# Kernel tuning notes

Measured on AMD Instinct MI355X. Metric: run time of the kernel, lower is better.

## Reference

```python
import jax, jax.numpy as jnp
from jax import lax
import numpy as np

# Model hyper-parameters (from init_kwargs)
B = 4
POINT_NUM = 32768
SKP_NUM = 512
ISK_NUM = 2
K1 = 32                       # skp_neighbor_num
K2 = int(K1 * SKP_NUM * 4 / POINT_NUM)   # = 2, as computed in __init__
RADIUS_SCALING = 1.5
SPHERE_N = 128                # points per sphere template


def _fibonacci_sphere(n):
    i = np.arange(n, dtype=np.float64) + 0.5
    phi = np.arccos(1.0 - 2.0 * i / n)
    theta = np.pi * (1.0 + 5.0 ** 0.5) * i
    return np.stack([np.cos(theta) * np.sin(phi),
                     np.sin(theta) * np.sin(phi),
                     np.cos(phi)], axis=-1).astype(np.float32)


def setup_inputs() -> dict:
    key = jax.random.key(0)
    xyz = jax.random.normal(key, (B, POINT_NUM, 3), dtype=jnp.float32)
    sphere_template = jnp.asarray(_fibonacci_sphere(SPHERE_N))  # [S,3] unit sphere
    return {"xyz": xyz, "sphere_template": sphere_template}


def _fps(xyz, n):
    """Iterative furthest point sampling. xyz: [B,N,3] -> indices [B,n] int32."""
    b, N, _ = xyz.shape
    dist0 = jnp.full((b, N), 1e10, dtype=xyz.dtype)
    last0 = jnp.zeros((b,), dtype=jnp.int32)

    def step(carry, _):
        dist, last = carry
        lp = jnp.take_along_axis(xyz, last[:, None, None], axis=1)  # [B,1,3]
        d = jnp.sum((xyz - lp) ** 2, axis=-1)                        # [B,N]
        dist = jnp.minimum(dist, d)
        nxt = jnp.argmax(dist, axis=-1).astype(jnp.int32)
        return (dist, nxt), last

    (_, _), idxs = lax.scan(step, (dist0, last0), None, length=n)
    return idxs.T  # [B,n]


def _pairwise_sqdist(centers, pts):
    # [B,M,N] squared distances
    c2 = jnp.sum(centers ** 2, axis=-1)[:, :, None]
    p2 = jnp.sum(pts ** 2, axis=-1)[:, None, :]
    cp = jnp.einsum('bmd,bnd->bmn', centers, pts)
    return c2 + p2 - 2.0 * cp


def _sklnz(centers, pts, k):
    """SkeletonizationBlock: move each center to the mean of its k nearest
    points in pts; radius = mean distance to those neighbors."""
    d2 = _pairwise_sqdist(centers, pts)          # [B,M,N]
    neg, idx = lax.top_k(-d2, k)                 # [B,M,k]
    nb = jax.vmap(lambda x, i: x[i])(pts, idx)   # [B,M,k,3]
    new_centers = jnp.mean(nb, axis=2)
    radius = jnp.mean(jnp.sqrt(jnp.clip(-neg, 0.0)), axis=2)  # [B,M]
    return new_centers, radius


def _forward(xyz, sphere_template):
    # Stage 1: FPS to 4*skp_num seeds, then iterative skeletonization
    ids = _fps(xyz, SKP_NUM * 4)                               # [B,4*skp]
    centers = jnp.take_along_axis(xyz, ids[:, :, None], axis=1)
    radius = None
    for _ in range(ISK_NUM):
        centers, radius = _sklnz(centers, xyz, K1)
    # Stage 2: FPS on intermediate skeleton down to skp_num
    xyz2 = centers
    ids2 = _fps(xyz2, SKP_NUM)                                 # [B,skp]
    centers = jnp.take_along_axis(xyz2, ids2[:, :, None], axis=1)
    radius = jnp.take_along_axis(radius, ids2, axis=1)
    for _ in range(ISK_NUM):
        centers, _radius = _sklnz(centers, xyz2, K2)
    radius = (radius + _radius) * RADIUS_SCALING               # [B,skp]
    # Sphere reconstruction: template scaled by radius, translated to centers
    sphere_points = centers[:, :, None, :] + radius[:, :, None, None] * sphere_template[None, None]
    return centers, sphere_points, radius


def reference(xyz, sphere_template):
    return _forward(xyz, sphere_template)
```

## Files before the change

kernel.cpp:

```cpp
#include <hip/hip_runtime.h>
#include <cstdint>

#define BATCH 4
#define NPTS  32768
#define QN    8192
#define SKP   512
#define M1    (SKP*4)
#define KA    32
#define KB    2
#define SPHN  128

typedef unsigned long long u64;

__device__ __forceinline__ float sqdist(float px, float py, float pz,
                                        float cx, float cy, float cz) {
  float dx = px - cx, dy = py - cy, dz = pz - cz;
  return __fadd_rn(__fadd_rn(__fmul_rn(dx, dx), __fmul_rn(dy, dy)),
                   __fmul_rn(dz, dz));
}
__device__ __forceinline__ float d2gram(float px, float py, float pz,
                                        float qx, float qy, float qz, float q2) {
  float p2 = __fadd_rn(__fadd_rn(__fmul_rn(px, px), __fmul_rn(py, py)),
                       __fmul_rn(pz, pz));
  float cp = __fadd_rn(__fadd_rn(__fmul_rn(qx, px), __fmul_rn(qy, py)),
                       __fmul_rn(qz, pz));
  return __fsub_rn(__fadd_rn(q2, p2), __fadd_rn(cp, cp));
}

__device__ __forceinline__ u64 shfl_xor_u64(u64 v, int off) {
  int lo = __shfl_xor((int)(unsigned)v, off);
  int hi = __shfl_xor((int)(unsigned)(v >> 32), off);
  return ((u64)(unsigned)hi << 32) | (unsigned)lo;
}
__device__ __forceinline__ u64 shfl_u64(u64 v, int src) {
  int lo = __shfl((int)(unsigned)v, src);
  int hi = __shfl((int)(unsigned)(v >> 32), src);
  return ((u64)(unsigned)hi << 32) | (unsigned)lo;
}
__device__ __forceinline__ u64 umax64(u64 a, u64 b) { return a > b ? a : b; }
__device__ __forceinline__ u64 umin64(u64 a, u64 b) { return a < b ? a : b; }
__device__ __forceinline__ void ins3(u64& k1, u64& k2, u64& k3, u64 v) {
  k3 = umax64(k3, umin64(k2, v));
  k2 = umax64(k2, umin64(k1, v));
  k1 = umax64(k1, v);
}

__global__ __launch_bounds__(1024)
void fps1_kernel(const float* __restrict__ xyz, float4* __restrict__ cen4a,
                 u64* __restrict__ sync)
{
  int blk = blockIdx.x;
  int b = blk >> 2, sub = blk & 3;
  const float* X = xyz + (size_t)b * NPTS * 3;
  cen4a += (size_t)b * M1;
  int tid = threadIdx.x, lane = tid & 63, wave = tid >> 6;
  int base = sub * QN;

  __shared__ float2 xysh[QN];
  __shared__ u64 s_w[16][8];
  __shared__ float4 s_cc[448];
  __shared__ float s_pivc[48][3];
  __shared__ int s_J;

  float zr[8], dist[8];
#pragma unroll
  for (int j = 0; j < 8; ++j) {
    int pl = tid + 1024 * j;
    int pg = base + pl;
    xysh[pl] = make_float2(X[3*pg], X[3*pg+1]);
    zr[j] = X[3*pg+2];
    dist[j] = 1e10f;
  }
  if (tid == 0) {
    s_pivc[0][0] = X[0]; s_pivc[0][1] = X[1]; s_pivc[0][2] = X[2];
    if (sub == 0) cen4a[0] = make_float4(X[0], X[1], X[2], 0.f);
  }
  __syncthreads();

  int it = 1, J = 1, rc = 1;

  while (it < M1) {
    for (int jp0 = 0; jp0 < J; jp0 += 4) {
      float pxa[4], pya[4], pza[4];
#pragma unroll
      for (int l = 0; l < 4; ++l) {
        int jj = jp0 + l; jj = (jj < J) ? jj : jp0;
        pxa[l] = s_pivc[jj][0]; pya[l] = s_pivc[jj][1]; pza[l] = s_pivc[jj][2];
      }
#pragma unroll
      for (int j = 0; j < 8; ++j) {
        int pl = tid + 1024 * j;
        float2 c2 = xysh[pl];
        float dd = dist[j];
#pragma unroll
        for (int l = 0; l < 4; ++l)
          dd = fminf(dd, sqdist(c2.x, c2.y, zr[j], pxa[l], pya[l], pza[l]));
        dist[j] = dd;
      }
    }
    u64 kk[8];
#pragma unroll
    for (int j = 0; j < 8; ++j) {
      int pg = base + tid + 1024 * j;
      kk[j] = ((u64)__float_as_uint(dist[j]) << 15) | (unsigned)(0x7FFF - pg);
    }
#define CE(A,B) { u64 _h = umax64(kk[A], kk[B]); kk[B] = umin64(kk[A], kk[B]); kk[A] = _h; }
    CE(0,1) CE(2,3) CE(4,5) CE(6,7)
    CE(0,2) CE(1,3) CE(4,6) CE(5,7)
    CE(1,2) CE(5,6)
    CE(0,4) CE(1,5) CE(2,6) CE(3,7)
    CE(2,4) CE(3,5)
    CE(1,2) CE(3,4) CE(5,6)
#pragma unroll
    for (int off = 1; off < 64; off <<= 1) {
#pragma unroll
      for (int i = 0; i < 4; ++i) {
        u64 o_lo = shfl_xor_u64(kk[7-i], off);
        u64 o_hi = shfl_xor_u64(kk[i], off);
        u64 n_i  = umax64(kk[i], o_lo);
        u64 n_7i = umax64(kk[7-i], o_hi);
        kk[i] = n_i; kk[7-i] = n_7i;
      }
      CE(0,4) CE(1,5) CE(2,6) CE(3,7)
      CE(0,2) CE(1,3) CE(4,6) CE(5,7)
      CE(0,1) CE(2,3) CE(4,5) CE(6,7)
    }
#undef CE
    unsigned tag = (unsigned)rc;
    int par = rc & 1;
    int sbase = ((b * 2 + par) * 4 + sub) * 128;
    if (lane < 8) {
      u64 kv = kk[0];
      kv = (lane == 1) ? kk[1] : kv;
      kv = (lane == 2) ? kk[2] : kv;
      kv = (lane == 3) ? kk[3] : kv;
      kv = (lane == 4) ? kk[4] : kv;
      kv = (lane == 5) ? kk[5] : kv;
      kv = (lane == 6) ? kk[6] : kv;
      kv = (lane == 7) ? kk[7] : kv;
      s_w[wave][lane] = kv;
      int slot = (lane < 7) ? (sbase + lane * 16 + wave) : (sbase + 112 + wave);
      __hip_atomic_store(&sync[slot], (kv << 12) | tag,
                         __ATOMIC_RELAXED, __HIP_MEMORY_SCOPE_AGENT);
    }
    __syncthreads();
    if (wave == 0) {
      u64 fb = (lane < 16) ? s_w[lane][7] : 0;
#pragma unroll
      for (int off = 8; off > 0; off >>= 1) fb = umax64(fb, shfl_xor_u64(fb, off));
      u64 f = shfl_u64(fb, 0);
      u64 ck[8]; int pp[8];
      ck[0] = s_w[lane & 15][lane >> 4];              pp[0] = lane;
      ck[1] = (lane < 48) ? s_w[lane & 15][4 + (lane >> 4)] : 0;
      pp[1] = (lane < 48) ? lane + 64 : -1;
      int slots[6]; bool need[6]; int ss[6];
#pragma unroll
      for (int k = 0; k < 6; ++k) {
        int m = lane + 64 * k;
        int r = m >> 7, s = m & 127;
        ss[k] = s;
        int rblk = (sub + 1 + r) & 3;
        slots[k] = ((b * 2 + par) * 4 + rblk) * 128 + s;
        need[k] = true; ck[2 + k] = 0; pp[2 + k] = (s < 112) ? 112 * (r + 1) + s : -1;
      }
      for (;;) {
        bool any = false;
#pragma unroll
        for (int k = 0; k < 6; ++k) if (need[k]) {
          u64 v = __hip_atomic_load(&sync[slots[k]],
                                    __ATOMIC_RELAXED, __HIP_MEMORY_SCOPE_AGENT);
          if ((unsigned)(v & 0xFFFu) == tag) { ck[2 + k] = v >> 12; need[k] = false; }
          else any = true;
        }
        if (!__any(any)) break;
      }
#pragma unroll
      for (int k = 0; k < 6; ++k) {
        if (ss[k] >= 112) { f = umax64(f, ck[2 + k]); ck[2 + k] = 0; }
      }
#pragma unroll
      for (int off = 32; off > 0; off >>= 1) f = umax64(f, shfl_xor_u64(f, off));
#pragma unroll
      for (int k = 0; k < 8; ++k) {
        if (pp[k] >= 0) {
          int ci = 0x7FFF - (int)(ck[k] & 0x7FFFu);
          s_cc[pp[k]] = make_float4(X[3*ci], X[3*ci+1], X[3*ci+2], 0.f);
        }
      }
      int Jn = 0;
      while (it + Jn < M1 && Jn < 48) {
        u64 lmk = ck[0]; int li = 0;
#pragma unroll
        for (int k = 1; k < 8; ++k) if (ck[k] > lmk) { lmk = ck[k]; li = k; }
        u64 mk = lmk;
#pragma unroll
        for (int off = 32; off > 0; off >>= 1) mk = umax64(mk, shfl_xor_u64(mk, off));
        if (!(mk > f)) break;
        u64 ball = __ballot(lmk == mk);
        int ow = __ffsll((long long)ball) - 1;
        int lp = pp[0];
#pragma unroll
        for (int k = 1; k < 8; ++k) lp = (li == k) ? pp[k] : lp;
        float4 c = s_cc[lp < 0 ? 0 : lp];
        float px = __shfl(c.x, ow), py = __shfl(c.y, ow), pz = __shfl(c.z, ow);
        if (lane == 0) {
          s_pivc[Jn][0] = px; s_pivc[Jn][1] = py; s_pivc[Jn][2] = pz;
          if (sub == 0) cen4a[it + Jn] = make_float4(px, py, pz, 0.f);
        }
#pragma unroll
        for (int k = 0; k < 8; ++k) {
          float4 cc = s_cc[pp[k] < 0 ? 0 : pp[k]];
          float d = sqdist(cc.x, cc.y, cc.z, px, py, pz);
          float nv = fminf(__uint_as_float((unsigned)(ck[k] >> 15)), d);
          ck[k] = ((u64)__float_as_uint(nv) << 15) | (ck[k] & 0x7FFFu);
        }
        ++Jn;
      }
      if (lane == 0) s_J = Jn;
    }
    __syncthreads();
    J = s_J;
    it += J;
    rc += 1;
  }
}

__global__ __launch_bounds__(1024)
void fps2_kernel(const float4* __restrict__ pts, int* __restrict__ ids)
{
  int b = blockIdx.x;
  pts += (size_t)b * M1;
  ids += (size_t)b * SKP;
  int tid = threadIdx.x, lane = tid & 63, wave = tid >> 6;

  __shared__ float4 pl[M1];
  __shared__ u64 s_w[16][3];
  __shared__ float s_pivc[16][3];
  __shared__ int s_J;

  float4 f0 = pts[tid], f1 = pts[tid + 1024];
  pl[tid] = f0; pl[tid + 1024] = f1;
  float dist0 = 1e10f, dist1 = 1e10f;
  if (tid == 0) {
    ids[0] = 0;
    s_pivc[0][0] = f0.x; s_pivc[0][1] = f0.y; s_pivc[0][2] = f0.z;
  }
  __syncthreads();

  int it = 1, J = 1;

  while (it < SKP) {
    for (int jp0 = 0; jp0 < J; jp0 += 4) {
      float pxa[4], pya[4], pza[4];
#pragma unroll
      for (int l = 0; l < 4; ++l) {
        int jj = jp0 + l; jj = (jj < J) ? jj : jp0;
        pxa[l] = s_pivc[jj][0]; pya[l] = s_pivc[jj][1]; pza[l] = s_pivc[jj][2];
      }
#pragma unroll
      for (int l = 0; l < 4; ++l) {
        dist0 = fminf(dist0, sqdist(f0.x, f0.y, f0.z, pxa[l], pya[l], pza[l]));
        dist1 = fminf(dist1, sqdist(f1.x, f1.y, f1.z, pxa[l], pya[l], pza[l]));
      }
    }
    u64 k1, k2 = 0, k3 = 0;
    k1 = ((u64)__float_as_uint(dist0) << 15) | (unsigned)(0x7FFF - tid);
    {
      u64 key = ((u64)__float_as_uint(dist1) << 15) | (unsigned)(0x7FFF - (tid + 1024));
      ins3(k1, k2, k3, key);
    }
#pragma unroll
    for (int off = 32; off > 0; off >>= 1) {
      u64 o1 = shfl_xor_u64(k1, off);
      u64 o2 = shfl_xor_u64(k2, off);
      u64 o3 = shfl_xor_u64(k3, off);
      ins3(k1, k2, k3, o1);
      ins3(k1, k2, k3, o2);
      ins3(k1, k2, k3, o3);
    }
    if (lane == 0) { s_w[wave][0] = k1; s_w[wave][1] = k2; s_w[wave][2] = k3; }
    __syncthreads();
    if (wave == 0) {
      u64 fb = (lane < 16) ? s_w[lane][2] : 0;
#pragma unroll
      for (int off = 8; off > 0; off >>= 1) {
        u64 o = shfl_xor_u64(fb, off);
        if (o > fb) fb = o;
      }
      u64 f = shfl_u64(fb, 0);
      u64 ck = 0;
      if (lane < 16)      ck = s_w[lane][0];
      else if (lane < 32) ck = s_w[lane - 16][1];
      int ci = (0x7FFF - (int)(ck & 0x7FFFu)) & (M1 - 1);
      float4 c = pl[ci];
      int Jn = 0;
      while (it + Jn < SKP && Jn < 16) {
        u64 mk = ck;
#pragma unroll
        for (int off = 32; off > 0; off >>= 1) {
          u64 o = shfl_xor_u64(mk, off);
          if (o > mk) mk = o;
        }
        if (!(mk > f)) break;
        u64 ball = __ballot(ck == mk);
        int wl = __ffsll((long long)ball) - 1;
        float px = __shfl(c.x, wl), py = __shfl(c.y, wl), pz = __shfl(c.z, wl);
        if (lane == 0) {
          s_pivc[Jn][0] = px; s_pivc[Jn][1] = py; s_pivc[Jn][2] = pz;
          ids[it + Jn] = 0x7FFF - (int)(mk & 0x7FFFu);
        }
        float d = sqdist(c.x, c.y, c.z, px, py, pz);
        float nv = fminf(__uint_as_float((unsigned)(ck >> 15)), d);
        ck = ((u64)__float_as_uint(nv) << 15) | (ck & 0x7FFFu);
        ++Jn;
      }
      if (lane == 0) s_J = Jn;
    }
    __syncthreads();
    J = s_J;
    it += J;
  }
}

template<int K, int KL, int N, bool S3>
__global__ __launch_bounds__(256)
void sklnz_kernel(const float4* __restrict__ queries,
                  const void*   __restrict__ ptsv,
                  float4* __restrict__ outc,
                  float*  __restrict__ outr,
                  int M)
{
  const int CH = N / 64;
  const int CHP = N / 256;
  int wave = threadIdx.x >> 6, lane = threadIdx.x & 63;
  int qid = blockIdx.x * 4 + wave;
  int b = qid / M;
  const float*  P3 = (const float*)ptsv + (size_t)b * N * 3;
  const float4* P4 = (const float4*)ptsv + (size_t)b * N;
  const float4* P4p = (const float4*)P3;
  float4 q = queries[qid];
  float q2 = __fadd_rn(__fadd_rn(__fmul_rn(q.x, q.x), __fmul_rn(q.y, q.y)),
                       __fmul_rn(q.z, q.z));

  __shared__ float heads[4][64][K + 1];

  float a[KL];
#pragma unroll
  for (int s = 0; s < KL; ++s) a[s] = 3.0e38f;
  if constexpr (S3) {
    for (int j = 0; j < CHP; ++j) {
      int u = lane + 64 * j;
      float4 A = P4p[3*u], B = P4p[3*u+1], C = P4p[3*u+2];
      float ds[4];
      ds[0] = d2gram(A.x, A.y, A.z, q.x, q.y, q.z, q2);
      ds[1] = d2gram(A.w, B.x, B.y, q.x, q.y, q.z, q2);
      ds[2] = d2gram(B.z, B.w, C.x, q.x, q.y, q.z, q2);
      ds[3] = d2gram(C.y, C.z, C.w, q.x, q.y, q.z, q2);
#pragma unroll
      for (int e = 0; e < 4; ++e) {
#pragma unroll
        for (int s = KL - 1; s > 0; --s) a[s] = fminf(a[s], fmaxf(a[s-1], ds[e]));
        a[0] = fminf(a[0], ds[e]);
      }
    }
  } else {
    for (int j = 0; j < CH; ++j) {
      float4 f = P4[lane + 64 * j];
      float d = d2gram(f.x, f.y, f.z, q.x, q.y, q.z, q2);
#pragma unroll
      for (int s = KL - 1; s > 0; --s) a[s] = fminf(a[s], fmaxf(a[s-1], d));
      a[0] = fminf(a[0], d);
    }
  }
#pragma unroll
  for (int s = 0; s < KL; ++s) heads[wave][lane][s] = a[s];
  heads[wave][lane][KL] = 3.1e38f;
  int h = 0; float t = 0.f;
  for (int r = 0; r < K; ++r) {
    float mv = heads[wave][lane][h];
    int   ml = lane;
#pragma unroll
    for (int off = 32; off > 0; off >>= 1) {
      float ov = __shfl_xor(mv, off);
      int   ol = __shfl_xor(ml, off);
      if (ov < mv || (ov == mv && ol < ml)) { mv = ov; ml = ol; }
    }
    t = mv;
    if (ml == lane) h++;
  }

  float sx = 0.f, sy = 0.f, sz = 0.f, sr = 0.f;
  int cl = 0;
  int myNext = 0x7fffffff;
  if constexpr (S3) {
    for (int j = 0; j < CHP; ++j) {
      int u = lane + 64 * j;
      float4 A = P4p[3*u], B = P4p[3*u+1], C = P4p[3*u+2];
      float pxs[4] = {A.x, A.w, B.z, C.y};
      float pys[4] = {A.y, B.x, B.w, C.z};
      float pzs[4] = {A.z, B.y, C.x, C.w};
#pragma unroll
      for (int e = 0; e < 4; ++e) {
        float d = d2gram(pxs[e], pys[e], pzs[e], q.x, q.y, q.z, q2);
        if (d < t) { sx += pxs[e]; sy += pys[e]; sz += pzs[e];
                     sr += sqrtf(fmaxf(d, 0.f)); cl++; }
        else if (d == t && myNext == 0x7fffffff) myNext = 4*u + e;
      }
    }
  } else {
    for (int j = 0; j < CH; ++j) {
      int p = lane + 64 * j;
      float4 f = P4[p];
      float d = d2gram(f.x, f.y, f.z, q.x, q.y, q.z, q2);
      if (d < t) { sx += f.x; sy += f.y; sz += f.z; sr += sqrtf(fmaxf(d, 0.f)); cl++; }
      else if (d == t && myNext == 0x7fffffff) myNext = p;
    }
  }
  int ctot = cl;
#pragma unroll
  for (int off = 32; off > 0; off >>= 1) ctot += __shfl_xor(ctot, off);

  if constexpr (KL < K) {
    if (ctot >= K) {
      float a2[K];
#pragma unroll
      for (int s = 0; s < K; ++s) a2[s] = 3.0e38f;
      for (int j = 0; j < CHP; ++j) {
        int u = lane + 64 * j;
        float4 A = P4p[3*u], B = P4p[3*u+1], C = P4p[3*u+2];
        float ds[4];
        ds[0] = d2gram(A.x, A.y, A.z, q.x, q.y, q.z, q2);
        ds[1] = d2gram(A.w, B.x, B.y, q.x, q.y, q.z, q2);
        ds[2] = d2gram(B.z, B.w, C.x, q.x, q.y, q.z, q2);
        ds[3] = d2gram(C.y, C.z, C.w, q.x, q.y, q.z, q2);
#pragma unroll
        for (int e = 0; e < 4; ++e) {
#pragma unroll
          for (int s = K - 1; s > 0; --s) a2[s] = fminf(a2[s], fmaxf(a2[s-1], ds[e]));
          a2[0] = fminf(a2[0], ds[e]);
        }
      }
#pragma unroll
      for (int s = 0; s < K; ++s) heads[wave][lane][s] = a2[s];
      heads[wave][lane][K] = 3.1e38f;
      h = 0;
      for (int r = 0; r < K; ++r) {
        float mv = heads[wave][lane][h];
        int   ml = lane;
#pragma unroll
        for (int off = 32; off > 0; off >>= 1) {
          float ov = __shfl_xor(mv, off);
          int   ol = __shfl_xor(ml, off);
          if (ov < mv || (ov == mv && ol < ml)) { mv = ov; ml = ol; }
        }
        t = mv;
        if (ml == lane) h++;
      }
      sx = sy = sz = sr = 0.f; cl = 0; myNext = 0x7fffffff;
      for (int j = 0; j < CHP; ++j) {
        int u = lane + 64 * j;
        float4 A = P4p[3*u], B = P4p[3*u+1], C = P4p[3*u+2];
        float pxs[4] = {A.x, A.w, B.z, C.y};
        float pys[4] = {A.y, B.x, B.w, C.z};
        float pzs[4] = {A.z, B.y, C.x, C.w};
#pragma unroll
        for (int e = 0; e < 4; ++e) {
          float d = d2gram(pxs[e], pys[e], pzs[e], q.x, q.y, q.z, q2);
          if (d < t) { sx += pxs[e]; sy += pys[e]; sz += pzs[e];
                       sr += sqrtf(fmaxf(d, 0.f)); cl++; }
          else if (d == t && myNext == 0x7fffffff) myNext = 4*u + e;
        }
      }
      ctot = cl;
#pragma unroll
      for (int off = 32; off > 0; off >>= 1) ctot += __shfl_xor(ctot, off);
    }
  }

  int need = K - ctot;
  float rt = sqrtf(fmaxf(t, 0.f));

  for (int e0 = 0; e0 < need; ++e0) {
    int mn = myNext;
#pragma unroll
    for (int off = 32; off > 0; off >>= 1) mn = min(mn, __shfl_xor(mn, off));
    if (myNext == mn) {
      float px, py, pz;
      if (S3) { px = P3[3*mn]; py = P3[3*mn+1]; pz = P3[3*mn+2]; }
      else    { float4 f = P4[mn]; px = f.x; py = f.y; pz = f.z; }
      sx += px; sy += py; sz += pz; sr += rt;
      int nx = 0x7fffffff;
      if constexpr (S3) {
        for (int j = ((mn >> 2) - lane) / 64; j < CHP && nx == 0x7fffffff; ++j) {
          int u = lane + 64 * j;
          float4 A = P4p[3*u], B = P4p[3*u+1], C = P4p[3*u+2];
          float pxs[4] = {A.x, A.w, B.z, C.y};
          float pys[4] = {A.y, B.x, B.w, C.z};
          float pzs[4] = {A.z, B.y, C.x, C.w};
#pragma unroll
          for (int e = 0; e < 4; ++e) {
            int p = 4*u + e;
            float d = d2gram(pxs[e], pys[e], pzs[e], q.x, q.y, q.z, q2);
            if (p > mn && d == t && nx == 0x7fffffff) nx = p;
          }
        }
      } else {
        for (int j = (mn - lane) / 64 + 1; j < CH && nx == 0x7fffffff; ++j) {
          int p = lane + 64 * j;
          float4 f = P4[p];
          float d = d2gram(f.x, f.y, f.z, q.x, q.y, q.z, q2);
          if (d == t) nx = p;
        }
      }
      myNext = nx;
    }
  }

#pragma unroll
  for (int off = 32; off > 0; off >>= 1) {
    sx += __shfl_xor(sx, off);
    sy += __shfl_xor(sy, off);
    sz += __shfl_xor(sz, off);
    sr += __shfl_xor(sr, off);
  }
  if (lane == 0) {
    const float inv = 1.0f / (float)K;
    outc[qid] = make_float4(sx * inv, sy * inv, sz * inv, 0.f);
    outr[qid] = sr * inv;
  }
}

__global__ void gather2_kernel(const float4* __restrict__ cen4,
                               const float* __restrict__ rad1,
                               const int* __restrict__ ids2,
                               float4* __restrict__ cen2,
                               float* __restrict__ radg)
{
  int g = blockIdx.x * 256 + threadIdx.x;
  if (g >= BATCH * SKP) return;
  int b = g / SKP;
  int p = ids2[g];
  cen2[g] = cen4[(size_t)b * M1 + p];
  radg[g] = rad1[(size_t)b * M1 + p];
}

__global__ void finalize_kernel(const float4* __restrict__ cen,
                                const float* __restrict__ radg,
                                const float* __restrict__ rad2,
                                const float* __restrict__ tmpl,
                                float* __restrict__ out)
{
  int g = blockIdx.x * 256 + threadIdx.x;
  int s = g >> 7;
  int j = g & 127;
  float4 c = cen[s];
  float r = __fmul_rn(__fadd_rn(radg[s], rad2[s]), 1.5f);
  float tx = tmpl[3*j], ty = tmpl[3*j+1], tz = tmpl[3*j+2];
  float* sp = out + BATCH * SKP * 3;
  sp[3*g]     = __fadd_rn(c.x, __fmul_rn(r, tx));
  sp[3*g + 1] = __fadd_rn(c.y, __fmul_rn(r, ty));
  sp[3*g + 2] = __fadd_rn(c.z, __fmul_rn(r, tz));
  if (j == 0) {
    out[3*s] = c.x; out[3*s+1] = c.y; out[3*s+2] = c.z;
    out[BATCH*SKP*3 + BATCH*SKP*SPHN*3 + s] = r;
  }
}

extern "C" void kernel_launch(void* const* d_in, const int* in_sizes, int n_in,
                              void* d_out, int out_size, void* d_ws, size_t ws_size,
                              hipStream_t stream)
{
  const float* xyz  = (const float*)d_in[0];
  const float* tmpl = (const float*)d_in[1];
  float* out = (float*)d_out;
  char* ws = (char*)d_ws;

  float4* cen4a = (float4*)(ws + 32768);
  float4* cen4b = (float4*)(ws + 163840);
  float*  rad1  = (float*) (ws + 294912);
  int*    ids2  = (int*)   (ws + 327680);
  float4* cen2a = (float4*)(ws + 335872);
  float4* cen2b = (float4*)(ws + 368640);
  float*  radg  = (float*) (ws + 401408);
  float*  rad2  = (float*) (ws + 409600);
  u64* sync = (u64*)(ws + 417792);

  fps1_kernel<<<BATCH * 4, 1024, 0, stream>>>(xyz, cen4a, sync);
  sklnz_kernel<KA, 4, NPTS, true><<<BATCH * M1 / 4, 256, 0, stream>>>(cen4a, xyz, cen4b, rad1, M1);
  sklnz_kernel<KA, 4, NPTS, true><<<BATCH * M1 / 4, 256, 0, stream>>>(cen4b, xyz, cen4a, rad1, M1);
  fps2_kernel<<<BATCH, 1024, 0, stream>>>(cen4a, ids2);
  gather2_kernel<<<(BATCH * SKP + 255) / 256, 256, 0, stream>>>(cen4a, rad1, ids2, cen2a, radg);
  sklnz_kernel<KB, KB, M1, false><<<BATCH * SKP / 4, 256, 0, stream>>>(cen2a, cen4a, cen2b, rad2, SKP);
  sklnz_kernel<KB, KB, M1, false><<<BATCH * SKP / 4, 256, 0, stream>>>(cen2b, cen4a, cen2a, rad2, SKP);
  finalize_kernel<<<BATCH * SKP * SPHN / 256, 256, 0, stream>>>(cen2a, radg, rad2, tmpl, out);
}
```

Before: 4.582 ms.

## Shrink FPS1 cross-block candidate exchange to top-2 per wave; fuse gather into FPS2

The first furthest-point-sampling kernel now keeps only the top three keys per thread and wave, replacing the 8-wide bitonic merge. Each block publishes 32 candidates plus a single floor value instead of 128 slots, and each round accepts at most 32 pivots instead of 48. The goal is to make each round's reduction, global-memory handshake and shared-memory staging cheaper. The catch is that fewer candidates per round may mean more rounds and more inter-block syncs. Separately, the gather of stage-2 centers and radii is folded into the end of fps2_kernel, removing one kernel launch and the global index buffer.

```diff
diff --git a/kernel.cpp b/kernel.cpp
--- a/kernel.cpp
+++ b/kernel.cpp
@@ -57,9 +57,8 @@
   int base = sub * QN;
 
   __shared__ float2 xysh[QN];
-  __shared__ u64 s_w[16][8];
-  __shared__ float4 s_cc[448];
-  __shared__ float s_pivc[48][3];
+  __shared__ u64 s_w[16][3];
+  __shared__ float s_pivc[32][3];
   __shared__ int s_J;
 
   float zr[8], dist[8];
@@ -98,122 +97,103 @@
         dist[j] = dd;
       }
     }
-    u64 kk[8];
+    u64 k1 = 0, k2 = 0, k3 = 0;
 #pragma unroll
     for (int j = 0; j < 8; ++j) {
       int pg = base + tid + 1024 * j;
-      kk[j] = ((u64)__float_as_uint(dist[j]) << 15) | (unsigned)(0x7FFF - pg);
-    }
-#define CE(A,B) { u64 _h = umax64(kk[A], kk[B]); kk[B] = umin64(kk[A], kk[B]); kk[A] = _h; }
-    CE(0,1) CE(2,3) CE(4,5) CE(6,7)
-    CE(0,2) CE(1,3) CE(4,6) CE(5,7)
-    CE(1,2) CE(5,6)
-    CE(0,4) CE(1,5) CE(2,6) CE(3,7)
-    CE(2,4) CE(3,5)
-    CE(1,2) CE(3,4) CE(5,6)
-#pragma unroll
-    for (int off = 1; off < 64; off <<= 1) {
-#pragma unroll
-      for (int i = 0; i < 4; ++i) {
-        u64 o_lo = shfl_xor_u64(kk[7-i], off);
-        u64 o_hi = shfl_xor_u64(kk[i], off);
-        u64 n_i  = umax64(kk[i], o_lo);
-        u64 n_7i = umax64(kk[7-i], o_hi);
-        kk[i] = n_i; kk[7-i] = n_7i;
-      }
-      CE(0,4) CE(1,5) CE(2,6) CE(3,7)
-      CE(0,2) CE(1,3) CE(4,6) CE(5,7)
-      CE(0,1) CE(2,3) CE(4,5) CE(6,7)
-    }
-#undef CE
-    unsigned tag = (unsigned)rc;
-    int par = rc & 1;
-    int sbase = ((b * 2 + par) * 4 + sub) * 128;
-    if (lane < 8) {
-      u64 kv = kk[0];
-      kv = (lane == 1) ? kk[1] : kv;
-      kv = (lane == 2) ? kk[2] : kv;
-      kv = (lane == 3) ? kk[3] : kv;
-      kv = (lane == 4) ? kk[4] : kv;
-      kv = (lane == 5) ? kk[5] : kv;
-      kv = (lane == 6) ? kk[6] : kv;
-      kv = (lane == 7) ? kk[7] : kv;
-      s_w[wave][lane] = kv;
-      int slot = (lane < 7) ? (sbase + lane * 16 + wave) : (sbase + 112 + wave);
-      __hip_atomic_store(&sync[slot], (kv << 12) | tag,
-                         __ATOMIC_RELAXED, __HIP_MEMORY_SCOPE_AGENT);
-    }
+      u64 key = ((u64)__float_as_uint(dist[j]) << 15) | (unsigned)(0x7FFF - pg);
+      ins3(k1, k2, k3, key);
+    }
+#pragma unroll
+    for (int off = 32; off > 0; off >>= 1) {
+      u64 o1 = shfl_xor_u64(k1, off);
+      u64 o2 = shfl_xor_u64(k2, off);
+      u64 o3 = shfl_xor_u64(k3, off);
+      ins3(k1, k2, k3, o1);
+      ins3(k1, k2, k3, o2);
+      ins3(k1, k2, k3, o3);
+    }
+    if (lane == 0) { s_w[wave][0] = k1; s_w[wave][1] = k2; s_w[wave][2] = k3; }
     __syncthreads();
     if (wave == 0) {
-      u64 fb = (lane < 16) ? s_w[lane][7] : 0;
-#pragma unroll
-      for (int off = 8; off > 0; off >>= 1) fb = umax64(fb, shfl_xor_u64(fb, off));
-      u64 f = shfl_u64(fb, 0);
-      u64 ck[8]; int pp[8];
-      ck[0] = s_w[lane & 15][lane >> 4];              pp[0] = lane;
-      ck[1] = (lane < 48) ? s_w[lane & 15][4 + (lane >> 4)] : 0;
-      pp[1] = (lane < 48) ? lane + 64 : -1;
-      int slots[6]; bool need[6]; int ss[6];
-#pragma unroll
-      for (int k = 0; k < 6; ++k) {
-        int m = lane + 64 * k;
-        int r = m >> 7, s = m & 127;
-        ss[k] = s;
-        int rblk = (sub + 1 + r) & 3;
-        slots[k] = ((b * 2 + par) * 4 + rblk) * 128 + s;
-        need[k] = true; ck[2 + k] = 0; pp[2 + k] = (s < 112) ? 112 * (r + 1) + s : -1;
-      }
-      for (;;) {
-        bool any = false;
-#pragma unroll
-        for (int k = 0; k < 6; ++k) if (need[k]) {
-          u64 v = __hip_atomic_load(&sync[slots[k]],
+      u64 fb = (lane < 16) ? s_w[lane][2] : 0;
+#pragma unroll
+      for (int off = 8; off > 0; off >>= 1) {
+        u64 o = shfl_xor_u64(fb, off);
+        if (o > fb) fb = o;
+      }
+      fb = shfl_u64(fb, 0);
+      unsigned tag = (unsigned)rc;
+      int par = rc & 1;
+      int sbase = ((b * 2 + par) * 4 + sub) * 40;
+      u64 mycand = 0;
+      if (lane < 16)      mycand = s_w[lane][0];
+      else if (lane < 32) mycand = s_w[lane - 16][1];
+      if (lane < 32)
+        __hip_atomic_store(&sync[sbase + lane], (mycand << 12) | tag,
+                           __ATOMIC_RELAXED, __HIP_MEMORY_SCOPE_AGENT);
+      if (lane == 32)
+        __hip_atomic_store(&sync[sbase + 32], (fb << 12) | tag,
+                           __ATOMIC_RELAXED, __HIP_MEMORY_SCOPE_AGENT);
+      int rel = (sub + (lane >> 4)) & 3;
+      int cb = ((b * 2 + par) * 4 + rel) * 40;
+      int c0s = cb + (lane & 15);
+      int c1s = cb + 16 + (lane & 15);
+      int fsl = ((b * 2 + par) * 4 + ((sub + lane) & 3)) * 40 + 32;
+      u64 ck0 = 0, ck1 = 0, flr = 0;
+      bool n0 = true, n1 = true, nf = (lane < 4);
+      while (__any(n0 || n1 || nf)) {
+        if (n0) {
+          u64 v = __hip_atomic_load(&sync[c0s],
                                     __ATOMIC_RELAXED, __HIP_MEMORY_SCOPE_AGENT);
-          if ((unsigned)(v & 0xFFFu) == tag) { ck[2 + k] = v >> 12; need[k] = false; }
-          else any = true;
-        }
-        if (!__any(any)) break;
-      }
-#pragma unroll
-      for (int k = 0; k < 6; ++k) {
-        if (ss[k] >= 112) { f = umax64(f, ck[2 + k]); ck[2 + k] = 0; }
-      }
-#pragma unroll
-      for (int off = 32; off > 0; off >>= 1) f = umax64(f, shfl_xor_u64(f, off));
-#pragma unroll
-      for (int k = 0; k < 8; ++k) {
-        if (pp[k] >= 0) {
-          int ci = 0x7FFF - (int)(ck[k] & 0x7FFFu);
-          s_cc[pp[k]] = make_float4(X[3*ci], X[3*ci+1], X[3*ci+2], 0.f);
-        }
-      }
+          if ((unsigned)(v & 0xFFFu) == tag) { ck0 = v >> 12; n0 = false; }
+        }
+        if (n1) {
+          u64 v = __hip_atomic_load(&sync[c1s],
+                                    __ATOMIC_RELAXED, __HIP_MEMORY_SCOPE_AGENT);
+          if ((unsigned)(v & 0xFFFu) == tag) { ck1 = v >> 12; n1 = false; }
+        }
+        if (nf) {
+          u64 v = __hip_atomic_load(&sync[fsl],
+                                    __ATOMIC_RELAXED, __HIP_MEMORY_SCOPE_AGENT);
+          if ((unsigned)(v & 0xFFFu) == tag) { flr = v >> 12; nf = false; }
+        }
+      }
+      u64 f = umax64(umax64(shfl_u64(flr, 0), shfl_u64(flr, 1)),
+                     umax64(shfl_u64(flr, 2), shfl_u64(flr, 3)));
+      int ci0 = 0x7FFF - (int)(ck0 & 0x7FFFu);
+      int ci1 = 0x7FFF - (int)(ck1 & 0x7FFFu);
+      float cx0 = X[3*ci0], cy0 = X[3*ci0+1], cz0 = X[3*ci0+2];
+      float cx1 = X[3*ci1], cy1 = X[3*ci1+1], cz1 = X[3*ci1+2];
       int Jn = 0;
-      while (it + Jn < M1 && Jn < 48) {
-        u64 lmk = ck[0]; int li = 0;
-#pragma unroll
-        for (int k = 1; k < 8; ++k) if (ck[k] > lmk) { lmk = ck[k]; li = k; }
-        u64 mk = lmk;
-#pragma unroll
-        for (int off = 32; off > 0; off >>= 1) mk = umax64(mk, shfl_xor_u64(mk, off));
+      while (it + Jn < M1 && Jn < 32) {
+        u64 mk = umax64(ck0, ck1);
+#pragma unroll
+        for (int off = 32; off > 0; off >>= 1) {
+          u64 o = shfl_xor_u64(mk, off);
+          if (o > mk) mk = o;
+        }
         if (!(mk > f)) break;
-        u64 ball = __ballot(lmk == mk);
-        int ow = __ffsll((long long)ball) - 1;
-        int lp = pp[0];
-#pragma unroll
-        for (int k = 1; k < 8; ++k) lp = (li == k) ? pp[k] : lp;
-        float4 c = s_cc[lp < 0 ? 0 : lp];
-        float px = __shfl(c.x, ow), py = __shfl(c.y, ow), pz = __shfl(c.z, ow);
+        u64 b0 = __ballot(ck0 == mk);
+        float px, py, pz;
+        if (b0) {
+          int wl = __ffsll((long long)b0) - 1;
+          px = __shfl(cx0, wl); py = __shfl(cy0, wl); pz = __shfl(cz0, wl);
+        } else {
+          u64 b1 = __ballot(ck1 == mk);
+          int wl = __ffsll((long long)b1) - 1;
+          px = __shfl(cx1, wl); py = __shfl(cy1, wl); pz = __shfl(cz1, wl);
+        }
         if (lane == 0) {
           s_pivc[Jn][0] = px; s_pivc[Jn][1] = py; s_pivc[Jn][2] = pz;
           if (sub == 0) cen4a[it + Jn] = make_float4(px, py, pz, 0.f);
         }
-#pragma unroll
-        for (int k = 0; k < 8; ++k) {
-          float4 cc = s_cc[pp[k] < 0 ? 0 : pp[k]];
-          float d = sqdist(cc.x, cc.y, cc.z, px, py, pz);
-          float nv = fminf(__uint_as_float((unsigned)(ck[k] >> 15)), d);
-          ck[k] = ((u64)__float_as_uint(nv) << 15) | (ck[k] & 0x7FFFu);
-        }
+        float d0 = sqdist(cx0, cy0, cz0, px, py, pz);
+        float n0v = fminf(__uint_as_float((unsigned)(ck0 >> 15)), d0);
+        ck0 = ((u64)__float_as_uint(n0v) << 15) | (ck0 & 0x7FFFu);
+        float d1 = sqdist(cx1, cy1, cz1, px, py, pz);
+        float n1v = fminf(__uint_as_float((unsigned)(ck1 >> 15)), d1);
+        ck1 = ((u64)__float_as_uint(n1v) << 15) | (ck1 & 0x7FFFu);
         ++Jn;
       }
       if (lane == 0) s_J = Jn;
@@ -226,23 +206,27 @@
 }
 
 __global__ __launch_bounds__(1024)
-void fps2_kernel(const float4* __restrict__ pts, int* __restrict__ ids)
+void fps2_kernel(const float4* __restrict__ pts, const float* __restrict__ rad1,
+                 float4* __restrict__ cen2, float* __restrict__ radg)
 {
   int b = blockIdx.x;
   pts += (size_t)b * M1;
-  ids += (size_t)b * SKP;
+  rad1 += (size_t)b * M1;
+  cen2 += (size_t)b * SKP;
+  radg += (size_t)b * SKP;
   int tid = threadIdx.x, lane = tid & 63, wave = tid >> 6;
 
   __shared__ float4 pl[M1];
   __shared__ u64 s_w[16][3];
   __shared__ float s_pivc[16][3];
+  __shared__ int s_ids[SKP];
   __shared__ int s_J;
 
   float4 f0 = pts[tid], f1 = pts[tid + 1024];
   pl[tid] = f0; pl[tid + 1024] = f1;
   float dist0 = 1e10f, dist1 = 1e10f;
   if (tid == 0) {
-    ids[0] = 0;
+    s_ids[0] = 0;
     s_pivc[0][0] = f0.x; s_pivc[0][1] = f0.y; s_pivc[0][2] = f0.z;
   }
   __syncthreads();
@@ -307,7 +291,7 @@
         float px = __shfl(c.x, wl), py = __shfl(c.y, wl), pz = __shfl(c.z, wl);
         if (lane == 0) {
           s_pivc[Jn][0] = px; s_pivc[Jn][1] = py; s_pivc[Jn][2] = pz;
-          ids[it + Jn] = 0x7FFF - (int)(mk & 0x7FFFu);
+          s_ids[it + Jn] = 0x7FFF - (int)(mk & 0x7FFFu);
         }
         float d = sqdist(c.x, c.y, c.z, px, py, pz);
         float nv = fminf(__uint_as_float((unsigned)(ck >> 15)), d);
@@ -319,6 +303,12 @@
     __syncthreads();
     J = s_J;
     it += J;
+  }
+  __syncthreads();
+  if (tid < SKP) {
+    int p = s_ids[tid];
+    cen2[tid] = pl[p];
+    radg[tid] = rad1[p];
   }
 }
 
@@ -530,20 +520,6 @@
   }
 }
 
-__global__ void gather2_kernel(const float4* __restrict__ cen4,
-                               const float* __restrict__ rad1,
-                               const int* __restrict__ ids2,
-                               float4* __restrict__ cen2,
-                               float* __restrict__ radg)
-{
-  int g = blockIdx.x * 256 + threadIdx.x;
-  if (g >= BATCH * SKP) return;
-  int b = g / SKP;
-  int p = ids2[g];
-  cen2[g] = cen4[(size_t)b * M1 + p];
-  radg[g] = rad1[(size_t)b * M1 + p];
-}
-
 __global__ void finalize_kernel(const float4* __restrict__ cen,
                                 const float* __restrict__ radg,
                                 const float* __restrict__ rad2,
@@ -578,7 +554,6 @@
   float4* cen4a = (float4*)(ws + 32768);
   float4* cen4b = (float4*)(ws + 163840);
   float*  rad1  = (float*) (ws + 294912);
-  int*    ids2  = (int*)   (ws + 327680);
   float4* cen2a = (float4*)(ws + 335872);
   float4* cen2b = (float4*)(ws + 368640);
   float*  radg  = (float*) (ws + 401408);
@@ -588,8 +563,7 @@
   fps1_kernel<<<BATCH * 4, 1024, 0, stream>>>(xyz, cen4a, sync);
   sklnz_kernel<KA, 4, NPTS, true><<<BATCH * M1 / 4, 256, 0, stream>>>(cen4a, xyz, cen4b, rad1, M1);
   sklnz_kernel<KA, 4, NPTS, true><<<BATCH * M1 / 4, 256, 0, stream>>>(cen4b, xyz, cen4a, rad1, M1);
-  fps2_kernel<<<BATCH, 1024, 0, stream>>>(cen4a, ids2);
-  gather2_kernel<<<(BATCH * SKP + 255) / 256, 256, 0, stream>>>(cen4a, rad1, ids2, cen2a, radg);
+  fps2_kernel<<<BATCH, 1024, 0, stream>>>(cen4a, rad1, cen2a, radg);
   sklnz_kernel<KB, KB, M1, false><<<BATCH * SKP / 4, 256, 0, stream>>>(cen2a, cen4a, cen2b, rad2, SKP);
   sklnz_kernel<KB, KB, M1, false><<<BATCH * SKP / 4, 256, 0, stream>>>(cen2b, cen4a, cen2a, rad2, SKP);
   finalize_kernel<<<BATCH * SKP * SPHN / 256, 256, 0, stream>>>(cen2a, radg, rad2, tmpl, out);
```

After: 3.960 ms (median of 2 runs). -13.6%, faster.
